# Kernel optimization log

Measured on AMD Instinct MI355X. Metric: run time of the kernel, lower is better.

The kernel has to match this reference:

```python
import jax, jax.numpy as jnp
import numpy as np

F = 50  # number of feature fields

def setup_inputs() -> dict:
    key = jax.random.key(0)
    k1, k2, k3, k4 = jax.random.split(key, 4)
    B, D, A = 4096, 16, 32
    return {
        "feat_emb": jax.random.normal(k1, (B, F, D), dtype=jnp.float32),
        "W": jax.random.normal(k2, (D, A), dtype=jnp.float32) * 0.1,
        "h": jax.random.normal(k3, (A,), dtype=jnp.float32),
        "p_vec": jax.random.normal(k4, (D,), dtype=jnp.float32),
    }

def reference(feat_emb, W, h, p_vec):
    # build_cross: upper-triangular field pairs (i < j)
    row, col = np.triu_indices(F, k=1)              # each [P], P = F*(F-1)/2
    p = feat_emb[:, row]                             # [B, P, D]
    q = feat_emb[:, col]                             # [B, P, D]
    inter = p * q                                    # pairwise interaction [B, P, D]
    # AttLayer: Dense(no bias) -> relu -> contract with h -> softmax over pairs
    att_signal = jax.nn.relu(jnp.einsum('bpd,da->bpa', inter, W))  # [B, P, A]
    scores = jnp.einsum('bpa,a->bp', att_signal, h)                # [B, P]
    att = jax.nn.softmax(scores, axis=1)                           # [B, P]
    # attention-weighted sum-pooling over pairs
    pooled = jnp.einsum('bp,bpd->bd', att, inter)                  # [B, D]
    # dropout omitted (inference); final projection and reduce
    out = jnp.einsum('bd,d->b', pooled, p_vec)[:, None]            # [B, 1]
    return out
```

## Files before the change

### kernel.cpp

```cpp
#include <hip/hip_runtime.h>
#include <math.h>


#define FF 50
#define DD 16
#define AA 32
#define NP 1225
#define NT 39
#define NTP 40
#define ERS 24
#define EBS (FF * ERS)
#define BPB 16
#define NTHR 512

typedef _Float16 half8 __attribute__((ext_vector_type(8)));
typedef _Float16 half4 __attribute__((ext_vector_type(4)));
typedef _Float16 half2v __attribute__((ext_vector_type(2)));
typedef __fp16   fh2    __attribute__((ext_vector_type(2)));
typedef float    floatx16 __attribute__((ext_vector_type(16)));

__global__ __launch_bounds__(NTHR, 4) void afm_kernel(
    const float* __restrict__ feat,
    const float* __restrict__ W,
    const float* __restrict__ h,
    const float* __restrict__ pvec,
    float* __restrict__ out,
    int Btot)
{
  __shared__ __align__(16) _Float16 eh[BPB * EBS];
  __shared__ unsigned int tbl[NTP * 32];

  const int tid    = threadIdx.x;
  const int lane   = tid & 63;
  const int wave   = tid >> 6;
  const int halfid = lane >> 5;
  const int n      = lane & 31;
  const int b0     = blockIdx.x * BPB;

  for (int s = tid; s < BPB * 200; s += NTHR) {
    int bl  = s / 200;
    int rem = s - bl * 200;
    int bb  = b0 + bl;
    if (bb < Btot) {
      float4 v4 = ((const float4*)feat)[(size_t)bb * 200 + rem];
      half4 hv;
      hv[0] = (_Float16)v4.x; hv[1] = (_Float16)v4.y;
      hv[2] = (_Float16)v4.z; hv[3] = (_Float16)v4.w;
      int row = rem >> 2, q = rem & 3;
      *(half4*)(&eh[bl * EBS + row * ERS + q * 4]) = hv;
    }
  }

  for (int q = tid; q < NTP * 32; q += NTHR) {
    int t = ((q >> 6) << 1) | (q & 1);
    int nn = (q >> 1) & 31;
    int p = t * 32 + nn;
    unsigned ent = 0;
    if (p < NP) {
      int rad = 9801 - 8 * p;
      int i = (int)((99.0f - sqrtf((float)rad)) * 0.5f);
      if (i < 0) i = 0; if (i > 48) i = 48;
      int off = (i * (99 - i)) >> 1;
      if (off > p) { --i; off = (i * (99 - i)) >> 1; }
      else {
        int off1 = ((i + 1) * (98 - i)) >> 1;
        if (off1 <= p) { ++i; off = off1; }
      }
      int j = p - off + i + 1;
      ent = ((unsigned)(i * 48) << 16) | (unsigned)(j * 48);
    }
    tbl[q] = ent;
  }

  const float LOG2E = 1.4426950408889634f;
  half8 A0;
  #pragma unroll
  for (int jj = 0; jj < 8; ++jj)
    A0[jj] = (_Float16)W[(halfid * 8 + jj) * AA + n];
  float hreg[16];
  #pragma unroll
  for (int r = 0; r < 16; ++r)
    hreg[r] = h[(r & 3) + 8 * (r >> 2) + 4 * halfid] * LOG2E;
  fh2 pv2[4];
  #pragma unroll
  for (int q = 0; q < 4; ++q) {
    pv2[q][0] = (__fp16)pvec[halfid * 8 + 2 * q];
    pv2[q][1] = (__fp16)pvec[halfid * 8 + 2 * q + 1];
  }
  const floatx16 ZACC = (floatx16)0.0f;

  __syncthreads();

  auto core = [&](const char* eb, unsigned oi, unsigned oj,
                  float& vout, float& gout) {
    half8 Bi = *(const half8*)(eb + oi);
    half8 Bj = *(const half8*)(eb + oj);
    half8 Bv = Bi * Bj;
    floatx16 z = __builtin_amdgcn_mfma_f32_32x32x16_f16(A0, Bv, ZACC, 0, 0, 0);
    float a0 = 0.f, a1 = 0.f, a2 = 0.f, a3 = 0.f;
    #pragma unroll
    for (int r = 0; r < 16; r += 4) {
      a0 = fmaf(fmaxf(z[r + 0], 0.f), hreg[r + 0], a0);
      a1 = fmaf(fmaxf(z[r + 1], 0.f), hreg[r + 1], a1);
      a2 = fmaf(fmaxf(z[r + 2], 0.f), hreg[r + 2], a2);
      a3 = fmaf(fmaxf(z[r + 3], 0.f), hreg[r + 3], a3);
    }
    float v = (a0 + a1) + (a2 + a3);
    vout = v + __shfl_xor(v, 32, 64);
#if __has_builtin(__builtin_amdgcn_fdot2)
    fh2 q0 = __builtin_bit_cast(fh2, (half2v)__builtin_shufflevector(Bv, Bv, 0, 1));
    fh2 q1 = __builtin_bit_cast(fh2, (half2v)__builtin_shufflevector(Bv, Bv, 2, 3));
    fh2 q2 = __builtin_bit_cast(fh2, (half2v)__builtin_shufflevector(Bv, Bv, 4, 5));
    fh2 q3 = __builtin_bit_cast(fh2, (half2v)__builtin_shufflevector(Bv, Bv, 6, 7));
    float gp0 = __builtin_amdgcn_fdot2(q1, pv2[1],
                __builtin_amdgcn_fdot2(q0, pv2[0], 0.f, false), false);
    float gp1 = __builtin_amdgcn_fdot2(q3, pv2[3],
                __builtin_amdgcn_fdot2(q2, pv2[2], 0.f, false), false);
    gout = gp0 + gp1;
#else
    float gp = 0.f;
    #pragma unroll
    for (int k = 0; k < 8; ++k)
      gp = fmaf((float)Bv[k], (float)((const __fp16*)&pv2[0])[k], gp);
    gout = gp;
#endif
  };

  const char* ebA = (const char*)(eh + (2 * wave) * EBS) + halfid * 16;
  const char* ebB = ebA + EBS * sizeof(_Float16);

  float denA = 0.f, numA = 0.f, denB = 0.f, numB = 0.f;
  const unsigned int* tpair = tbl + 2 * n;

  for (int th = 0; th < 19; ++th) {
    uint2 ij2 = *(const uint2*)(tpair + th * 64);
    unsigned oi0 = ij2.x >> 16, oj0 = ij2.x & 0xffffu;
    unsigned oi1 = ij2.y >> 16, oj1 = ij2.y & 0xffffu;
    float v, g;
    core(ebA, oi0, oj0, v, g);
    { float e = exp2f(v); denA += e; numA = fmaf(e, g, numA); }
    core(ebB, oi0, oj0, v, g);
    { float e = exp2f(v); denB += e; numB = fmaf(e, g, numB); }
    core(ebA, oi1, oj1, v, g);
    { float e = exp2f(v); denA += e; numA = fmaf(e, g, numA); }
    core(ebB, oi1, oj1, v, g);
    { float e = exp2f(v); denB += e; numB = fmaf(e, g, numB); }
  }
  {
    unsigned ij = tpair[19 * 64];
    unsigned oi = ij >> 16, oj = ij & 0xffffu;
    float v, g;
    core(ebA, oi, oj, v, g);
    if (n >= 9) v = -3.0e38f;
    { float e = exp2f(v); denA += e; numA = fmaf(e, g, numA); }
    core(ebB, oi, oj, v, g);
    if (n >= 9) v = -3.0e38f;
    { float e = exp2f(v); denB += e; numB = fmaf(e, g, numB); }
  }

  #pragma unroll
  for (int mask = 32; mask >= 1; mask >>= 1) {
    denA += __shfl_xor(denA, mask, 64);
    numA += __shfl_xor(numA, mask, 64);
    denB += __shfl_xor(denB, mask, 64);
    numB += __shfl_xor(numB, mask, 64);
  }
  const int bA = b0 + 2 * wave;
  if (lane == 0 && bA < Btot)     out[bA]     = (2.0f * numA) / denA;
  if (lane == 0 && bA + 1 < Btot) out[bA + 1] = (2.0f * numB) / denB;
}

extern "C" void kernel_launch(void* const* d_in, const int* in_sizes, int n_in,
                              void* d_out, int out_size, void* d_ws, size_t ws_size,
                              hipStream_t stream) {
  const float* feat = (const float*)d_in[0];
  const float* W    = (const float*)d_in[1];
  const float* h    = (const float*)d_in[2];
  const float* pvec = (const float*)d_in[3];
  float* out = (float*)d_out;
  const int B = in_sizes[0] / (FF * DD);
  afm_kernel<<<(B + BPB - 1) / BPB, NTHR, 0, stream>>>(feat, W, h, pvec, out, B);
}
```

Measured before the change: 87.27 us.

## Stage per-pair scores in LDS and run softmax reduction as a separate pass

Each wave now handles one batch row instead of two, and the block covers half as many rows. Per-pair score and projection values are combined across half-waves, written to shared memory, and then reduced with exp2 in a second pass using all 64 lanes. This removes the redundant exp/accumulate work that was duplicated across the two half-waves. In exchange it adds a large shared-memory buffer, lowers the occupancy hint, doubles the number of blocks and so repeats the table setup more often, and loses the interleaving of two independent rows per wave.

Measured after the change: 96.25 us. 10.3% more time.

```diff
diff --git a/kernel.cpp b/kernel.cpp
--- a/kernel.cpp
+++ b/kernel.cpp
@@ -10,8 +10,9 @@
 #define NTP 40
 #define ERS 24
 #define EBS (FF * ERS)
-#define BPB 16
+#define BPB 8
 #define NTHR 512
+#define SGN (NT * 32)
 
 typedef _Float16 half8 __attribute__((ext_vector_type(8)));
 typedef _Float16 half4 __attribute__((ext_vector_type(4)));
@@ -19,7 +20,7 @@
 typedef __fp16   fh2    __attribute__((ext_vector_type(2)));
 typedef float    floatx16 __attribute__((ext_vector_type(16)));
 
-__global__ __launch_bounds__(NTHR, 4) void afm_kernel(
+__global__ __launch_bounds__(NTHR, 2) void afm_kernel(
     const float* __restrict__ feat,
     const float* __restrict__ W,
     const float* __restrict__ h,
@@ -29,6 +30,7 @@
 {
   __shared__ __align__(16) _Float16 eh[BPB * EBS];
   __shared__ unsigned int tbl[NTP * 32];
+  __shared__ __align__(16) float2 sg[BPB * SGN];
 
   const int tid    = threadIdx.x;
   const int lane   = tid & 63;
@@ -91,8 +93,11 @@
 
   __syncthreads();
 
-  auto core = [&](const char* eb, unsigned oi, unsigned oj,
-                  float& vout, float& gout) {
+  const char* eb = (const char*)(eh + wave * EBS) + halfid * 16;
+  float2* sgw = sg + wave * SGN;
+  const unsigned int* tpair = tbl + 2 * n;
+
+  auto core = [&](unsigned oi, unsigned oj, float& vout, float& gout) {
     half8 Bi = *(const half8*)(eb + oi);
     half8 Bj = *(const half8*)(eb + oj);
     half8 Bv = Bi * Bj;
@@ -106,68 +111,57 @@
       a3 = fmaf(fmaxf(z[r + 3], 0.f), hreg[r + 3], a3);
     }
     float v = (a0 + a1) + (a2 + a3);
-    vout = v + __shfl_xor(v, 32, 64);
 #if __has_builtin(__builtin_amdgcn_fdot2)
     fh2 q0 = __builtin_bit_cast(fh2, (half2v)__builtin_shufflevector(Bv, Bv, 0, 1));
     fh2 q1 = __builtin_bit_cast(fh2, (half2v)__builtin_shufflevector(Bv, Bv, 2, 3));
     fh2 q2 = __builtin_bit_cast(fh2, (half2v)__builtin_shufflevector(Bv, Bv, 4, 5));
     fh2 q3 = __builtin_bit_cast(fh2, (half2v)__builtin_shufflevector(Bv, Bv, 6, 7));
-    float gp0 = __builtin_amdgcn_fdot2(q1, pv2[1],
-                __builtin_amdgcn_fdot2(q0, pv2[0], 0.f, false), false);
-    float gp1 = __builtin_amdgcn_fdot2(q3, pv2[3],
-                __builtin_amdgcn_fdot2(q2, pv2[2], 0.f, false), false);
-    gout = gp0 + gp1;
+    float g = __builtin_amdgcn_fdot2(q1, pv2[1],
+              __builtin_amdgcn_fdot2(q0, pv2[0], 0.f, false), false)
+            + __builtin_amdgcn_fdot2(q3, pv2[3],
+              __builtin_amdgcn_fdot2(q2, pv2[2], 0.f, false), false);
 #else
-    float gp = 0.f;
+    float g = 0.f;
     #pragma unroll
     for (int k = 0; k < 8; ++k)
-      gp = fmaf((float)Bv[k], (float)((const __fp16*)&pv2[0])[k], gp);
-    gout = gp;
+      g = fmaf((float)Bv[k], (float)((const __fp16*)pv2)[k], g);
 #endif
+    vout = v + __shfl_xor(v, 32, 64);
+    gout = g + __shfl_xor(g, 32, 64);
   };
-
-  const char* ebA = (const char*)(eh + (2 * wave) * EBS) + halfid * 16;
-  const char* ebB = ebA + EBS * sizeof(_Float16);
-
-  float denA = 0.f, numA = 0.f, denB = 0.f, numB = 0.f;
-  const unsigned int* tpair = tbl + 2 * n;
 
   for (int th = 0; th < 19; ++th) {
     uint2 ij2 = *(const uint2*)(tpair + th * 64);
-    unsigned oi0 = ij2.x >> 16, oj0 = ij2.x & 0xffffu;
-    unsigned oi1 = ij2.y >> 16, oj1 = ij2.y & 0xffffu;
-    float v, g;
-    core(ebA, oi0, oj0, v, g);
-    { float e = exp2f(v); denA += e; numA = fmaf(e, g, numA); }
-    core(ebB, oi0, oj0, v, g);
-    { float e = exp2f(v); denB += e; numB = fmaf(e, g, numB); }
-    core(ebA, oi1, oj1, v, g);
-    { float e = exp2f(v); denA += e; numA = fmaf(e, g, numA); }
-    core(ebB, oi1, oj1, v, g);
-    { float e = exp2f(v); denB += e; numB = fmaf(e, g, numB); }
+    float v0, g0, v1, g1;
+    core(ij2.x >> 16, ij2.x & 0xffffu, v0, g0);
+    core(ij2.y >> 16, ij2.y & 0xffffu, v1, g1);
+    if (lane < 32) {
+      sgw[(2 * th)     * 32 + n] = make_float2(v0, g0);
+      sgw[(2 * th + 1) * 32 + n] = make_float2(v1, g1);
+    }
   }
   {
     unsigned ij = tpair[19 * 64];
-    unsigned oi = ij >> 16, oj = ij & 0xffffu;
     float v, g;
-    core(ebA, oi, oj, v, g);
+    core(ij >> 16, ij & 0xffffu, v, g);
     if (n >= 9) v = -3.0e38f;
-    { float e = exp2f(v); denA += e; numA = fmaf(e, g, numA); }
-    core(ebB, oi, oj, v, g);
-    if (n >= 9) v = -3.0e38f;
-    { float e = exp2f(v); denB += e; numB = fmaf(e, g, numB); }
+    if (lane < 32) sgw[38 * 32 + n] = make_float2(v, g);
   }
 
+  float den = 0.f, num = 0.f;
+  for (int p = lane; p < SGN; p += 64) {
+    float2 s2 = sgw[p];
+    float e = exp2f(s2.x);
+    den += e;
+    num = fmaf(e, s2.y, num);
+  }
   #pragma unroll
   for (int mask = 32; mask >= 1; mask >>= 1) {
-    denA += __shfl_xor(denA, mask, 64);
-    numA += __shfl_xor(numA, mask, 64);
-    denB += __shfl_xor(denB, mask, 64);
-    numB += __shfl_xor(numB, mask, 64);
+    den += __shfl_xor(den, mask, 64);
+    num += __shfl_xor(num, mask, 64);
   }
-  const int bA = b0 + 2 * wave;
-  if (lane == 0 && bA < Btot)     out[bA]     = (2.0f * numA) / denA;
-  if (lane == 0 && bA + 1 < Btot) out[bA + 1] = (2.0f * numB) / denB;
+  const int b = b0 + wave;
+  if (lane == 0 && b < Btot) out[b] = num / den;
 }
 
 extern "C" void kernel_launch(void* const* d_in, const int* in_sizes, int n_in,
```
